# Optimization experiments

Hardware: AMD Instinct MI355X
Metric: run time of the kernel (lower is better)

## Reference

```python
import jax, jax.numpy as jnp
import numpy as np

B, I, A_IN = 32, 32, 16     # batch, input capsules, input atoms
OD, OA = 10, 16             # output_dim (classes), output_atoms
H, W = 12, 12               # spatial grid
NUM_ROUTING = 3


def _squash(t):
    # squash over atom dim (axis=2): x/|x| * |x|^2/(1+|x|^2) = x*|x|/(1+|x|^2)
    norm = jnp.linalg.norm(t, axis=2, keepdims=True)
    return t * norm / (1.0 + norm * norm)


def setup_inputs() -> dict:
    key = jax.random.key(0)
    k1, k2 = jax.random.split(key)
    x = jax.random.normal(k1, (B, I, A_IN, H, W), dtype=jnp.float32)
    # torch weight: (I, A_IN, OD*OA, 1, 1), init N(0, 0.1)
    weight = 0.1 * jax.random.normal(k2, (I, A_IN, OD * OA), dtype=jnp.float32)
    # torch bias: (OD, OA, 1, 1), init const 0.1
    bias = jnp.full((OD, OA, 1, 1), 0.1, dtype=jnp.float32)
    return {"x": x, "weight": weight, "bias": bias}


def reference(x, weight, bias):
    # votes: sum over input atoms -> [B, I, OD*OA, H, W] -> [B, I, OD, OA, H, W]
    votes = jnp.einsum("biahw,iak->bikhw", x, weight)
    votes = votes.reshape(B, I, OD, OA, H, W)
    biases = jnp.broadcast_to(bias, (OD, OA, H, W))

    # Dynamic routing. In the original, logits carry no gradient (built from
    # .data), so intermediate iterations are fully stop-gradient.
    votes_sg = jax.lax.stop_gradient(votes)
    logits = jnp.zeros((B, I, OD, H, W), dtype=votes.dtype)
    activation = None
    for i in range(NUM_ROUTING):
        route = jax.nn.softmax(logits, axis=2)  # softmax over output_dim
        v = votes if i == NUM_ROUTING - 1 else votes_sg
        preact = jnp.einsum("bidhw,bidahw->bdahw", route, v) + biases
        activation = _squash(preact)  # [B, OD, OA, H, W]
        if i < NUM_ROUTING - 1:
            # agreement (dot over atoms) updates logits
            logits = logits + jnp.einsum(
                "bidahw,bdahw->bidhw", votes_sg, jax.lax.stop_gradient(activation)
            )
    return activation
```

## Files before the change

### kernel.cpp

```cpp
#include <hip/hip_runtime.h>
#include <math.h>

#define NB 32
#define NI 32
#define NA 16
#define NOD 10
#define NOA 16
#define NK 160
#define NHW 144
#define NROUT 3
#define P 2
#define NTHREADS 512
#define SVLD 168

__device__ __forceinline__ unsigned short f2bf(float f) {
    unsigned b = __builtin_bit_cast(unsigned, f);
    b += 0x7fffu + ((b >> 16) & 1u);
    return (unsigned short)(b >> 16);
}
__device__ __forceinline__ float bf2f(unsigned short u) {
    return __builtin_bit_cast(float, (unsigned)u << 16);
}
__device__ __forceinline__ float bf_lo(unsigned d) {
    return __builtin_bit_cast(float, d << 16);
}
__device__ __forceinline__ float bf_hi(unsigned d) {
    return __builtin_bit_cast(float, d & 0xffff0000u);
}

__global__ __launch_bounds__(NTHREADS)
void capsule_routing_kernel(const float* __restrict__ x,
                            const float* __restrict__ weight,
                            const float* __restrict__ bias,
                            float* __restrict__ out)
{
    __shared__ float sx[NI][NA][P];
    __shared__ unsigned short sv[P * NI * SVLD];
    __shared__ float slog[P][NI][NOD];
    __shared__ float srt[P][NI][NOD];
    __shared__ float sact[P][NOD][NOA];

    const int bk  = blockIdx.x;
    const int b   = bk / (NHW / P);
    const int hw0 = (bk % (NHW / P)) * P;
    const int tid = threadIdx.x;

#define SVIDX(p, i, k) (((p) * NI + (i)) * SVLD + (k))

    if (tid < NI * NA) {
        const int i = tid >> 4;
        const int a = tid & (NA - 1);
        const float2 v = *reinterpret_cast<const float2*>(
            x + (size_t)((b * NI + i) * NA + a) * NHW + hw0);
        sx[i][a][0] = v.x;
        sx[i][a][1] = v.y;
    }
    {
        float* lf = &slog[0][0][0];
        for (int j = tid; j < P * NI * NOD; j += NTHREADS) lf[j] = 0.0f;
    }
    __syncthreads();

    for (int j = tid; j < NI * (NK / 4); j += NTHREADS) {
        const int i  = j / (NK / 4);
        const int k0 = (j - i * (NK / 4)) * 4;
        const float4* wp = reinterpret_cast<const float4*>(
            weight + (size_t)i * NA * NK + k0);
        float4 a0 = make_float4(0.f, 0.f, 0.f, 0.f);
        float4 a1 = make_float4(0.f, 0.f, 0.f, 0.f);
#pragma unroll
        for (int a = 0; a < NA; ++a) {
            const float4 w4 = wp[a * (NK / 4)];
            const float2 xa = *reinterpret_cast<const float2*>(&sx[i][a][0]);
            a0.x = fmaf(xa.x, w4.x, a0.x); a0.y = fmaf(xa.x, w4.y, a0.y);
            a0.z = fmaf(xa.x, w4.z, a0.z); a0.w = fmaf(xa.x, w4.w, a0.w);
            a1.x = fmaf(xa.y, w4.x, a1.x); a1.y = fmaf(xa.y, w4.y, a1.y);
            a1.z = fmaf(xa.y, w4.z, a1.z); a1.w = fmaf(xa.y, w4.w, a1.w);
        }
        ushort4 s0 = make_ushort4(f2bf(a0.x), f2bf(a0.y), f2bf(a0.z), f2bf(a0.w));
        ushort4 s1 = make_ushort4(f2bf(a1.x), f2bf(a1.y), f2bf(a1.z), f2bf(a1.w));
        *reinterpret_cast<ushort4*>(&sv[SVIDX(0, i, k0)]) = s0;
        *reinterpret_cast<ushort4*>(&sv[SVIDX(1, i, k0)]) = s1;
    }
    __syncthreads();

    for (int it = 0; it < NROUT; ++it) {
        if (tid < P * NI) {
            const int p = tid >> 5;
            const int i = tid & 31;
            float m = slog[p][i][0];
#pragma unroll
            for (int od = 1; od < NOD; ++od) m = fmaxf(m, slog[p][i][od]);
            float e[NOD];
            float s = 0.0f;
#pragma unroll
            for (int od = 0; od < NOD; ++od) {
                e[od] = __expf(slog[p][i][od] - m);
                s += e[od];
            }
            const float inv = 1.0f / s;
#pragma unroll
            for (int od = 0; od < NOD; ++od) srt[p][i][od] = e[od] * inv;
        }
        __syncthreads();

        if (tid < P * NK) {
            const int p  = tid / NK;
            const int k  = tid - p * NK;
            const int od = k >> 4;
            const int oa = k & (NOA - 1);
            float acc = bias[k];
            const unsigned short* svp = &sv[SVIDX(p, 0, k)];
#pragma unroll
            for (int i = 0; i < NI; ++i)
                acc = fmaf(srt[p][i][od], bf2f(svp[i * SVLD]), acc);
            float ss = acc * acc;
#pragma unroll
            for (int m = 1; m < NOA; m <<= 1)
                ss += __shfl_xor(ss, m, NOA);
            const float scale = sqrtf(ss) / (1.0f + ss);
            sact[p][od][oa] = acc * scale;
        }
        __syncthreads();

        if (it < NROUT - 1) {
            for (int j = tid; j < P * NI * NOD; j += NTHREADS) {
                const int p  = j / (NI * NOD);
                const int r  = j - p * (NI * NOD);
                const int od = r >> 5;
                const int i  = r & 31;
                const uint4 d0 = *reinterpret_cast<const uint4*>(
                    &sv[SVIDX(p, i, od * NOA)]);
                const uint4 d1 = *reinterpret_cast<const uint4*>(
                    &sv[SVIDX(p, i, od * NOA + 8)]);
                const float* ap = &sact[p][od][0];
                float acc;
                acc  = bf_lo(d0.x) * ap[0];
                acc = fmaf(bf_hi(d0.x), ap[1], acc);
                acc = fmaf(bf_lo(d0.y), ap[2], acc);
                acc = fmaf(bf_hi(d0.y), ap[3], acc);
                acc = fmaf(bf_lo(d0.z), ap[4], acc);
                acc = fmaf(bf_hi(d0.z), ap[5], acc);
                acc = fmaf(bf_lo(d0.w), ap[6], acc);
                acc = fmaf(bf_hi(d0.w), ap[7], acc);
                acc = fmaf(bf_lo(d1.x), ap[8], acc);
                acc = fmaf(bf_hi(d1.x), ap[9], acc);
                acc = fmaf(bf_lo(d1.y), ap[10], acc);
                acc = fmaf(bf_hi(d1.y), ap[11], acc);
                acc = fmaf(bf_lo(d1.z), ap[12], acc);
                acc = fmaf(bf_hi(d1.z), ap[13], acc);
                acc = fmaf(bf_lo(d1.w), ap[14], acc);
                acc = fmaf(bf_hi(d1.w), ap[15], acc);
                slog[p][i][od] += acc;
            }
            __syncthreads();
        }
    }

    __syncthreads();
    if (tid < NK) {
        const int od = tid >> 4;
        const int oa = tid & (NOA - 1);
        const float2 v = make_float2(sact[0][od][oa], sact[1][od][oa]);
        *reinterpret_cast<float2*>(out + (size_t)(b * NK + tid) * NHW + hw0) = v;
    }
}

extern "C" void kernel_launch(void* const* d_in, const int* in_sizes, int n_in,
                              void* d_out, int out_size, void* d_ws, size_t ws_size,
                              hipStream_t stream) {
    const float* x      = (const float*)d_in[0];
    const float* weight = (const float*)d_in[1];
    const float* bias   = (const float*)d_in[2];
    float* out          = (float*)d_out;

    const int nblocks = NB * (NHW / P);
    capsule_routing_kernel<<<nblocks, NTHREADS, 0, stream>>>(x, weight, bias, out);
}
```

Before: 47.92 us.

## Split vote computation into separate kernel writing bf16 votes to workspace

Splits the fused kernel in two. A votes kernel computes all votes once per (capsule, batch, half-grid), loading each weight slice into shared memory and writing bf16 votes to the workspace. A routing kernel then reads four spatial positions per block and keeps the routing logits in registers. This removes the redundant per-block weight reads of the fused version, but adds a global round trip of about 47 MB of bf16 votes and a second launch. A fallback to the original fused kernel is kept for when the workspace is too small.

```diff
diff --git a/kernel.cpp b/kernel.cpp
--- a/kernel.cpp
+++ b/kernel.cpp
@@ -9,9 +9,8 @@
 #define NK 160
 #define NHW 144
 #define NROUT 3
-#define P 2
-#define NTHREADS 512
-#define SVLD 168
+#define NROWS (NB*NHW)
+#define VOTES_BYTES ((size_t)NI * NROWS * NK * 2)
 
 __device__ __forceinline__ unsigned short f2bf(float f) {
     unsigned b = __builtin_bit_cast(unsigned, f);
@@ -28,24 +27,194 @@
     return __builtin_bit_cast(float, d & 0xffff0000u);
 }
 
-__global__ __launch_bounds__(NTHREADS)
-void capsule_routing_kernel(const float* __restrict__ x,
-                            const float* __restrict__ weight,
-                            const float* __restrict__ bias,
-                            float* __restrict__ out)
+__global__ __launch_bounds__(256)
+void votes_kernel(const float* __restrict__ x,
+                  const float* __restrict__ weight,
+                  unsigned short* __restrict__ votes)
 {
-    __shared__ float sx[NI][NA][P];
+    __shared__ float sw[NA * NK];
+    __shared__ float sxv[NA * 72];
+
+    const int i   = blockIdx.x >> 6;
+    const int b   = (blockIdx.x >> 1) & 31;
+    const int hw0 = (blockIdx.x & 1) * 72;
+    const int tid = threadIdx.x;
+
+    {
+        const float4* src = reinterpret_cast<const float4*>(weight + (size_t)i * NA * NK);
+        float4* dst = reinterpret_cast<float4*>(sw);
+        for (int j = tid; j < NA * NK / 4; j += 256) dst[j] = src[j];
+    }
+    {
+        const float* xb = x + ((size_t)(b * NI + i) * NA) * NHW + hw0;
+        for (int j = tid; j < NA * 18; j += 256) {
+            const int a = j / 18, c = j % 18;
+            *reinterpret_cast<float4*>(&sxv[a * 72 + c * 4]) =
+                *reinterpret_cast<const float4*>(xb + a * NHW + c * 4);
+        }
+    }
+    __syncthreads();
+
+    unsigned short* vbase = votes + ((size_t)i * NROWS + b * NHW + hw0) * NK;
+    for (int t = tid; t < 72 * 40; t += 256) {
+        const int kq  = (t >> 2) % 40;
+        const int hwl = (t & 3) + ((t / 160) << 2);
+        const int k0  = kq * 4;
+        float4 acc = make_float4(0.f, 0.f, 0.f, 0.f);
+#pragma unroll
+        for (int a = 0; a < NA; ++a) {
+            const float  xv = sxv[a * 72 + hwl];
+            const float4 w4 = *reinterpret_cast<const float4*>(&sw[a * NK + k0]);
+            acc.x = fmaf(xv, w4.x, acc.x);
+            acc.y = fmaf(xv, w4.y, acc.y);
+            acc.z = fmaf(xv, w4.z, acc.z);
+            acc.w = fmaf(xv, w4.w, acc.w);
+        }
+        const ushort4 s = make_ushort4(f2bf(acc.x), f2bf(acc.y), f2bf(acc.z), f2bf(acc.w));
+        *reinterpret_cast<ushort4*>(vbase + (size_t)hwl * NK + k0) = s;
+    }
+}
+
+#define P 4
+#define SVLD 168
+
+__global__ __launch_bounds__(512)
+void routing_kernel(const unsigned short* __restrict__ votes,
+                    const float* __restrict__ bias,
+                    float* __restrict__ out)
+{
     __shared__ unsigned short sv[P * NI * SVLD];
-    __shared__ float slog[P][NI][NOD];
     __shared__ float srt[P][NI][NOD];
     __shared__ float sact[P][NOD][NOA];
 
+    const int row0 = blockIdx.x * P;
+    const int tid  = threadIdx.x;
+
+    {
+        const uint4* src = reinterpret_cast<const uint4*>(votes);
+        for (int u = tid; u < NI * P * 20; u += 512) {
+            const int i = u / (P * 20);
+            const int r = u % (P * 20);
+            const int p = r / 20;
+            const int c = r % 20;
+            *reinterpret_cast<uint4*>(&sv[(p * NI + i) * SVLD + c * 8]) =
+                src[(size_t)(i * NROWS + row0 + p) * 20 + c];
+        }
+    }
+
+    float lg[NOD];
+#pragma unroll
+    for (int od = 0; od < NOD; ++od) lg[od] = 0.f;
+    const int pown = tid >> 5;
+    const int iown = tid & 31;
+    __syncthreads();
+
+    for (int it = 0; it < NROUT; ++it) {
+        if (tid < P * NI) {
+            float m = lg[0];
+#pragma unroll
+            for (int od = 1; od < NOD; ++od) m = fmaxf(m, lg[od]);
+            float e[NOD];
+            float s = 0.f;
+#pragma unroll
+            for (int od = 0; od < NOD; ++od) {
+                e[od] = __expf(lg[od] - m);
+                s += e[od];
+            }
+            const float inv = 1.f / s;
+#pragma unroll
+            for (int od = 0; od < NOD; ++od) srt[pown][iown][od] = e[od] * inv;
+        }
+        __syncthreads();
+
+        for (int j = tid; j < P * NK; j += 512) {
+            const int p  = j / NK;
+            const int k  = j - p * NK;
+            const int od = k >> 4;
+            const int oa = k & 15;
+            float acc = bias[k];
+            const unsigned short* svp = &sv[p * NI * SVLD + k];
+#pragma unroll
+            for (int i = 0; i < NI; ++i)
+                acc = fmaf(srt[p][i][od], bf2f(svp[i * SVLD]), acc);
+            float ss = acc * acc;
+#pragma unroll
+            for (int m = 1; m < NOA; m <<= 1)
+                ss += __shfl_xor(ss, m, NOA);
+            const float scale = sqrtf(ss) / (1.f + ss);
+            sact[p][od][oa] = acc * scale;
+        }
+        __syncthreads();
+
+        if (it < NROUT - 1) {
+            for (int j = tid; j < P * NI * NOD; j += 512) {
+                const int p  = j / (NI * NOD);
+                const int r  = j - p * (NI * NOD);
+                const int od = r >> 5;
+                const int i  = r & 31;
+                const uint4 d0 = *reinterpret_cast<const uint4*>(
+                    &sv[(p * NI + i) * SVLD + od * NOA]);
+                const uint4 d1 = *reinterpret_cast<const uint4*>(
+                    &sv[(p * NI + i) * SVLD + od * NOA + 8]);
+                const float* ap = &sact[p][od][0];
+                float acc;
+                acc  = bf_lo(d0.x) * ap[0];
+                acc = fmaf(bf_hi(d0.x), ap[1], acc);
+                acc = fmaf(bf_lo(d0.y), ap[2], acc);
+                acc = fmaf(bf_hi(d0.y), ap[3], acc);
+                acc = fmaf(bf_lo(d0.z), ap[4], acc);
+                acc = fmaf(bf_hi(d0.z), ap[5], acc);
+                acc = fmaf(bf_lo(d0.w), ap[6], acc);
+                acc = fmaf(bf_hi(d0.w), ap[7], acc);
+                acc = fmaf(bf_lo(d1.x), ap[8], acc);
+                acc = fmaf(bf_hi(d1.x), ap[9], acc);
+                acc = fmaf(bf_lo(d1.y), ap[10], acc);
+                acc = fmaf(bf_hi(d1.y), ap[11], acc);
+                acc = fmaf(bf_lo(d1.z), ap[12], acc);
+                acc = fmaf(bf_hi(d1.z), ap[13], acc);
+                acc = fmaf(bf_lo(d1.w), ap[14], acc);
+                acc = fmaf(bf_hi(d1.w), ap[15], acc);
+                srt[p][i][od] = acc;
+            }
+            __syncthreads();
+            if (tid < P * NI) {
+#pragma unroll
+                for (int od = 0; od < NOD; ++od) lg[od] += srt[pown][iown][od];
+            }
+        }
+    }
+
+    if (tid < NK) {
+        const int b  = row0 / NHW;
+        const int hw = row0 % NHW;
+        const int od = tid >> 4;
+        const int oa = tid & 15;
+        const float4 v = make_float4(sact[0][od][oa], sact[1][od][oa],
+                                     sact[2][od][oa], sact[3][od][oa]);
+        *reinterpret_cast<float4*>(out + ((size_t)b * NK + tid) * NHW + hw) = v;
+    }
+}
+
+#define FP 2
+#define FSVLD 168
+
+__global__ __launch_bounds__(512)
+void capsule_fallback_kernel(const float* __restrict__ x,
+                             const float* __restrict__ weight,
+                             const float* __restrict__ bias,
+                             float* __restrict__ out)
+{
+    __shared__ float sx[NI][NA][FP];
+    __shared__ unsigned short sv[FP * NI * FSVLD];
+    __shared__ float slog[FP][NI][NOD];
+    __shared__ float srt[FP][NI][NOD];
+    __shared__ float sact[FP][NOD][NOA];
+
     const int bk  = blockIdx.x;
-    const int b   = bk / (NHW / P);
-    const int hw0 = (bk % (NHW / P)) * P;
+    const int b   = bk / (NHW / FP);
+    const int hw0 = (bk % (NHW / FP)) * FP;
     const int tid = threadIdx.x;
-
-#define SVIDX(p, i, k) (((p) * NI + (i)) * SVLD + (k))
+#define FSVIDX(p, i, k) (((p) * NI + (i)) * FSVLD + (k))
 
     if (tid < NI * NA) {
         const int i = tid >> 4;
@@ -57,15 +226,14 @@
     }
     {
         float* lf = &slog[0][0][0];
-        for (int j = tid; j < P * NI * NOD; j += NTHREADS) lf[j] = 0.0f;
-    }
-    __syncthreads();
-
-    for (int j = tid; j < NI * (NK / 4); j += NTHREADS) {
+        for (int j = tid; j < FP * NI * NOD; j += 512) lf[j] = 0.0f;
+    }
+    __syncthreads();
+
+    for (int j = tid; j < NI * (NK / 4); j += 512) {
         const int i  = j / (NK / 4);
         const int k0 = (j - i * (NK / 4)) * 4;
-        const float4* wp = reinterpret_cast<const float4*>(
-            weight + (size_t)i * NA * NK + k0);
+        const float4* wp = reinterpret_cast<const float4*>(weight + (size_t)i * NA * NK + k0);
         float4 a0 = make_float4(0.f, 0.f, 0.f, 0.f);
         float4 a1 = make_float4(0.f, 0.f, 0.f, 0.f);
 #pragma unroll
@@ -79,13 +247,13 @@
         }
         ushort4 s0 = make_ushort4(f2bf(a0.x), f2bf(a0.y), f2bf(a0.z), f2bf(a0.w));
         ushort4 s1 = make_ushort4(f2bf(a1.x), f2bf(a1.y), f2bf(a1.z), f2bf(a1.w));
-        *reinterpret_cast<ushort4*>(&sv[SVIDX(0, i, k0)]) = s0;
-        *reinterpret_cast<ushort4*>(&sv[SVIDX(1, i, k0)]) = s1;
+        *reinterpret_cast<ushort4*>(&sv[FSVIDX(0, i, k0)]) = s0;
+        *reinterpret_cast<ushort4*>(&sv[FSVIDX(1, i, k0)]) = s1;
     }
     __syncthreads();
 
     for (int it = 0; it < NROUT; ++it) {
-        if (tid < P * NI) {
+        if (tid < FP * NI) {
             const int p = tid >> 5;
             const int i = tid & 31;
             float m = slog[p][i][0];
@@ -104,16 +272,16 @@
         }
         __syncthreads();
 
-        if (tid < P * NK) {
+        if (tid < FP * NK) {
             const int p  = tid / NK;
             const int k  = tid - p * NK;
             const int od = k >> 4;
             const int oa = k & (NOA - 1);
             float acc = bias[k];
-            const unsigned short* svp = &sv[SVIDX(p, 0, k)];
+            const unsigned short* svp = &sv[FSVIDX(p, 0, k)];
 #pragma unroll
             for (int i = 0; i < NI; ++i)
-                acc = fmaf(srt[p][i][od], bf2f(svp[i * SVLD]), acc);
+                acc = fmaf(srt[p][i][od], bf2f(svp[i * FSVLD]), acc);
             float ss = acc * acc;
 #pragma unroll
             for (int m = 1; m < NOA; m <<= 1)
@@ -124,15 +292,13 @@
         __syncthreads();
 
         if (it < NROUT - 1) {
-            for (int j = tid; j < P * NI * NOD; j += NTHREADS) {
+            for (int j = tid; j < FP * NI * NOD; j += 512) {
                 const int p  = j / (NI * NOD);
                 const int r  = j - p * (NI * NOD);
                 const int od = r >> 5;
                 const int i  = r & 31;
-                const uint4 d0 = *reinterpret_cast<const uint4*>(
-                    &sv[SVIDX(p, i, od * NOA)]);
-                const uint4 d1 = *reinterpret_cast<const uint4*>(
-                    &sv[SVIDX(p, i, od * NOA + 8)]);
+                const uint4 d0 = *reinterpret_cast<const uint4*>(&sv[FSVIDX(p, i, od * NOA)]);
+                const uint4 d1 = *reinterpret_cast<const uint4*>(&sv[FSVIDX(p, i, od * NOA + 8)]);
                 const float* ap = &sact[p][od][0];
                 float acc;
                 acc  = bf_lo(d0.x) * ap[0];
@@ -174,6 +340,11 @@
     const float* bias   = (const float*)d_in[2];
     float* out          = (float*)d_out;
 
-    const int nblocks = NB * (NHW / P);
-    capsule_routing_kernel<<<nblocks, NTHREADS, 0, stream>>>(x, weight, bias, out);
-}
+    if (ws_size >= VOTES_BYTES) {
+        unsigned short* votes = (unsigned short*)d_ws;
+        votes_kernel<<<NI * NB * 2, 256, 0, stream>>>(x, weight, votes);
+        routing_kernel<<<NROWS / P, 512, 0, stream>>>(votes, bias, out);
+    } else {
+        capsule_fallback_kernel<<<NB * (NHW / FP), 512, 0, stream>>>(x, weight, bias, out);
+    }
+}
```

New measurement: 62.60 us. +30.6%, slower.

## Assign one wavefront per spatial position and route with wave-level sync

Applied to the files above, without the earlier changes.

Each block now handles 4 spatial positions with 256 threads, one 64-lane wave per position. Routing logits live in registers and every routing step syncs with wave barriers instead of block-wide __syncthreads. The vote computation reuses each weight load across 4 positions instead of 2, which halves weight traffic per output. The risk is fewer blocks, and wave-barrier correctness relies on each wave touching only its own shared-memory slices.

```diff
diff --git a/kernel.cpp b/kernel.cpp
--- a/kernel.cpp
+++ b/kernel.cpp
@@ -9,8 +9,7 @@
 #define NK 160
 #define NHW 144
 #define NROUT 3
-#define P 2
-#define NTHREADS 512
+#define NROWS (NB*NHW)
 #define SVLD 168
 
 __device__ __forceinline__ unsigned short f2bf(float f) {
@@ -18,9 +17,6 @@
     b += 0x7fffu + ((b >> 16) & 1u);
     return (unsigned short)(b >> 16);
 }
-__device__ __forceinline__ float bf2f(unsigned short u) {
-    return __builtin_bit_cast(float, (unsigned)u << 16);
-}
 __device__ __forceinline__ float bf_lo(unsigned d) {
     return __builtin_bit_cast(float, d << 16);
 }
@@ -28,141 +24,181 @@
     return __builtin_bit_cast(float, d & 0xffff0000u);
 }
 
-__global__ __launch_bounds__(NTHREADS)
-void capsule_routing_kernel(const float* __restrict__ x,
-                            const float* __restrict__ weight,
-                            const float* __restrict__ bias,
-                            float* __restrict__ out)
+__global__ __launch_bounds__(256)
+void capsule_fused_kernel(const float* __restrict__ x,
+                          const float* __restrict__ weight,
+                          const float* __restrict__ bias,
+                          float* __restrict__ out)
 {
-    __shared__ float sx[NI][NA][P];
-    __shared__ unsigned short sv[P * NI * SVLD];
-    __shared__ float slog[P][NI][NOD];
-    __shared__ float srt[P][NI][NOD];
-    __shared__ float sact[P][NOD][NOA];
-
-    const int bk  = blockIdx.x;
-    const int b   = bk / (NHW / P);
-    const int hw0 = (bk % (NHW / P)) * P;
-    const int tid = threadIdx.x;
-
-#define SVIDX(p, i, k) (((p) * NI + (i)) * SVLD + (k))
-
-    if (tid < NI * NA) {
-        const int i = tid >> 4;
-        const int a = tid & (NA - 1);
-        const float2 v = *reinterpret_cast<const float2*>(
-            x + (size_t)((b * NI + i) * NA + a) * NHW + hw0);
-        sx[i][a][0] = v.x;
-        sx[i][a][1] = v.y;
-    }
+    __shared__ unsigned short sv[4][NI][SVLD];
+    __shared__ __align__(16) float pool[2048];
+    float* const srt_f  = pool;
+    float* const sact_f = pool + 4 * NOD * 33;
+
+    const int tid  = threadIdx.x;
+    const int w    = tid >> 6;
+    const int l    = tid & 63;
+    const int b    = blockIdx.x / (NHW / 4);
+    const int hw0  = (blockIdx.x % (NHW / 4)) * 4;
+
     {
-        float* lf = &slog[0][0][0];
-        for (int j = tid; j < P * NI * NOD; j += NTHREADS) lf[j] = 0.0f;
+        const float* xb = x + ((size_t)b * NI * NA) * NHW + hw0;
+        for (int j = tid; j < NI * NA; j += 256) {
+            const float4 v = *reinterpret_cast<const float4*>(xb + (size_t)j * NHW);
+            *reinterpret_cast<float4*>(&pool[j * 4]) = v;
+        }
     }
     __syncthreads();
 
-    for (int j = tid; j < NI * (NK / 4); j += NTHREADS) {
-        const int i  = j / (NK / 4);
-        const int k0 = (j - i * (NK / 4)) * 4;
+    for (int j = tid; j < NI * 40; j += 256) {
+        const int i  = j / 40;
+        const int kq = j - i * 40;
+        const int k0 = kq * 4;
         const float4* wp = reinterpret_cast<const float4*>(
             weight + (size_t)i * NA * NK + k0);
         float4 a0 = make_float4(0.f, 0.f, 0.f, 0.f);
         float4 a1 = make_float4(0.f, 0.f, 0.f, 0.f);
+        float4 a2 = make_float4(0.f, 0.f, 0.f, 0.f);
+        float4 a3 = make_float4(0.f, 0.f, 0.f, 0.f);
 #pragma unroll
         for (int a = 0; a < NA; ++a) {
-            const float4 w4 = wp[a * (NK / 4)];
-            const float2 xa = *reinterpret_cast<const float2*>(&sx[i][a][0]);
+            const float4 w4 = wp[(size_t)a * 40];
+            const float4 xa = *reinterpret_cast<const float4*>(&pool[(i * NA + a) * 4]);
             a0.x = fmaf(xa.x, w4.x, a0.x); a0.y = fmaf(xa.x, w4.y, a0.y);
             a0.z = fmaf(xa.x, w4.z, a0.z); a0.w = fmaf(xa.x, w4.w, a0.w);
             a1.x = fmaf(xa.y, w4.x, a1.x); a1.y = fmaf(xa.y, w4.y, a1.y);
             a1.z = fmaf(xa.y, w4.z, a1.z); a1.w = fmaf(xa.y, w4.w, a1.w);
-        }
-        ushort4 s0 = make_ushort4(f2bf(a0.x), f2bf(a0.y), f2bf(a0.z), f2bf(a0.w));
-        ushort4 s1 = make_ushort4(f2bf(a1.x), f2bf(a1.y), f2bf(a1.z), f2bf(a1.w));
-        *reinterpret_cast<ushort4*>(&sv[SVIDX(0, i, k0)]) = s0;
-        *reinterpret_cast<ushort4*>(&sv[SVIDX(1, i, k0)]) = s1;
-    }
+            a2.x = fmaf(xa.z, w4.x, a2.x); a2.y = fmaf(xa.z, w4.y, a2.y);
+            a2.z = fmaf(xa.z, w4.z, a2.z); a2.w = fmaf(xa.z, w4.w, a2.w);
+            a3.x = fmaf(xa.w, w4.x, a3.x); a3.y = fmaf(xa.w, w4.y, a3.y);
+            a3.z = fmaf(xa.w, w4.z, a3.z); a3.w = fmaf(xa.w, w4.w, a3.w);
+        }
+        *reinterpret_cast<ushort4*>(&sv[0][i][k0]) =
+            make_ushort4(f2bf(a0.x), f2bf(a0.y), f2bf(a0.z), f2bf(a0.w));
+        *reinterpret_cast<ushort4*>(&sv[1][i][k0]) =
+            make_ushort4(f2bf(a1.x), f2bf(a1.y), f2bf(a1.z), f2bf(a1.w));
+        *reinterpret_cast<ushort4*>(&sv[2][i][k0]) =
+            make_ushort4(f2bf(a2.x), f2bf(a2.y), f2bf(a2.z), f2bf(a2.w));
+        *reinterpret_cast<ushort4*>(&sv[3][i][k0]) =
+            make_ushort4(f2bf(a3.x), f2bf(a3.y), f2bf(a3.z), f2bf(a3.w));
+    }
+
+    const float2 b0 = *reinterpret_cast<const float2*>(bias + 2 * l);
+    float2 b1 = make_float2(0.f, 0.f);
+    if (l < 16) b1 = *reinterpret_cast<const float2*>(bias + 128 + 2 * l);
+
+    float lg[NOD];
+#pragma unroll
+    for (int od = 0; od < NOD; ++od) lg[od] = 0.f;
+    const int iown = l & 31;
+
     __syncthreads();
 
     for (int it = 0; it < NROUT; ++it) {
-        if (tid < P * NI) {
-            const int p = tid >> 5;
-            const int i = tid & 31;
-            float m = slog[p][i][0];
-#pragma unroll
-            for (int od = 1; od < NOD; ++od) m = fmaxf(m, slog[p][i][od]);
+        {
+            float m = lg[0];
+#pragma unroll
+            for (int od = 1; od < NOD; ++od) m = fmaxf(m, lg[od]);
             float e[NOD];
-            float s = 0.0f;
+            float s = 0.f;
 #pragma unroll
             for (int od = 0; od < NOD; ++od) {
-                e[od] = __expf(slog[p][i][od] - m);
+                e[od] = __expf(lg[od] - m);
                 s += e[od];
             }
-            const float inv = 1.0f / s;
-#pragma unroll
-            for (int od = 0; od < NOD; ++od) srt[p][i][od] = e[od] * inv;
-        }
-        __syncthreads();
-
-        if (tid < P * NK) {
-            const int p  = tid / NK;
-            const int k  = tid - p * NK;
-            const int od = k >> 4;
-            const int oa = k & (NOA - 1);
-            float acc = bias[k];
-            const unsigned short* svp = &sv[SVIDX(p, 0, k)];
-#pragma unroll
-            for (int i = 0; i < NI; ++i)
-                acc = fmaf(srt[p][i][od], bf2f(svp[i * SVLD]), acc);
-            float ss = acc * acc;
-#pragma unroll
-            for (int m = 1; m < NOA; m <<= 1)
-                ss += __shfl_xor(ss, m, NOA);
-            const float scale = sqrtf(ss) / (1.0f + ss);
-            sact[p][od][oa] = acc * scale;
-        }
-        __syncthreads();
+            const float inv = 1.f / s;
+            if (l < 32) {
+#pragma unroll
+                for (int od = 0; od < NOD; ++od)
+                    srt_f[(w * NOD + od) * 33 + iown] = e[od] * inv;
+            }
+        }
+        __builtin_amdgcn_wave_barrier();
+
+        {
+            const int od0 = l >> 3;
+            float a0 = b0.x, a1 = b0.y;
+#pragma unroll
+            for (int i = 0; i < NI; ++i) {
+                const unsigned d = *reinterpret_cast<const unsigned*>(&sv[w][i][2 * l]);
+                const float r = srt_f[(w * NOD + od0) * 33 + i];
+                a0 = fmaf(r, bf_lo(d), a0);
+                a1 = fmaf(r, bf_hi(d), a1);
+            }
+            float ss = a0 * a0 + a1 * a1;
+            ss += __shfl_xor(ss, 1, 8);
+            ss += __shfl_xor(ss, 2, 8);
+            ss += __shfl_xor(ss, 4, 8);
+            const float sc = sqrtf(ss) / (1.f + ss);
+            *reinterpret_cast<float2*>(&sact_f[w * 164 + 2 * l]) =
+                make_float2(a0 * sc, a1 * sc);
+
+            if (l < 16) {
+                const int od1 = 8 + (l >> 3);
+                float c0 = b1.x, c1 = b1.y;
+#pragma unroll
+                for (int i = 0; i < NI; ++i) {
+                    const unsigned d = *reinterpret_cast<const unsigned*>(&sv[w][i][128 + 2 * l]);
+                    const float r = srt_f[(w * NOD + od1) * 33 + i];
+                    c0 = fmaf(r, bf_lo(d), c0);
+                    c1 = fmaf(r, bf_hi(d), c1);
+                }
+                float s2 = c0 * c0 + c1 * c1;
+                s2 += __shfl_xor(s2, 1, 8);
+                s2 += __shfl_xor(s2, 2, 8);
+                s2 += __shfl_xor(s2, 4, 8);
+                const float sc2 = sqrtf(s2) / (1.f + s2);
+                *reinterpret_cast<float2*>(&sact_f[w * 164 + 128 + 2 * l]) =
+                    make_float2(c0 * sc2, c1 * sc2);
+            }
+        }
+        __builtin_amdgcn_wave_barrier();
 
         if (it < NROUT - 1) {
-            for (int j = tid; j < P * NI * NOD; j += NTHREADS) {
-                const int p  = j / (NI * NOD);
-                const int r  = j - p * (NI * NOD);
-                const int od = r >> 5;
-                const int i  = r & 31;
-                const uint4 d0 = *reinterpret_cast<const uint4*>(
-                    &sv[SVIDX(p, i, od * NOA)]);
-                const uint4 d1 = *reinterpret_cast<const uint4*>(
-                    &sv[SVIDX(p, i, od * NOA + 8)]);
-                const float* ap = &sact[p][od][0];
+#pragma unroll
+            for (int r = 0; r < 5; ++r) {
+                const int t  = l + 64 * r;
+                const int i  = t & 31;
+                const int od = t >> 5;
+                const uint4 d0 = *reinterpret_cast<const uint4*>(&sv[w][i][od * NOA]);
+                const uint4 d1 = *reinterpret_cast<const uint4*>(&sv[w][i][od * NOA + 8]);
+                const float* ap = &sact_f[w * 164 + od * NOA];
+                const float4 c0 = *reinterpret_cast<const float4*>(ap + 0);
+                const float4 c1 = *reinterpret_cast<const float4*>(ap + 4);
+                const float4 c2 = *reinterpret_cast<const float4*>(ap + 8);
+                const float4 c3 = *reinterpret_cast<const float4*>(ap + 12);
                 float acc;
-                acc  = bf_lo(d0.x) * ap[0];
-                acc = fmaf(bf_hi(d0.x), ap[1], acc);
-                acc = fmaf(bf_lo(d0.y), ap[2], acc);
-                acc = fmaf(bf_hi(d0.y), ap[3], acc);
-                acc = fmaf(bf_lo(d0.z), ap[4], acc);
-                acc = fmaf(bf_hi(d0.z), ap[5], acc);
-                acc = fmaf(bf_lo(d0.w), ap[6], acc);
-                acc = fmaf(bf_hi(d0.w), ap[7], acc);
-                acc = fmaf(bf_lo(d1.x), ap[8], acc);
-                acc = fmaf(bf_hi(d1.x), ap[9], acc);
-                acc = fmaf(bf_lo(d1.y), ap[10], acc);
-                acc = fmaf(bf_hi(d1.y), ap[11], acc);
-                acc = fmaf(bf_lo(d1.z), ap[12], acc);
-                acc = fmaf(bf_hi(d1.z), ap[13], acc);
-                acc = fmaf(bf_lo(d1.w), ap[14], acc);
-                acc = fmaf(bf_hi(d1.w), ap[15], acc);
-                slog[p][i][od] += acc;
-            }
-            __syncthreads();
+                acc  = bf_lo(d0.x) * c0.x;
+                acc = fmaf(bf_hi(d0.x), c0.y, acc);
+                acc = fmaf(bf_lo(d0.y), c0.z, acc);
+                acc = fmaf(bf_hi(d0.y), c0.w, acc);
+                acc = fmaf(bf_lo(d0.z), c1.x, acc);
+                acc = fmaf(bf_hi(d0.z), c1.y, acc);
+                acc = fmaf(bf_lo(d0.w), c1.z, acc);
+                acc = fmaf(bf_hi(d0.w), c1.w, acc);
+                acc = fmaf(bf_lo(d1.x), c2.x, acc);
+                acc = fmaf(bf_hi(d1.x), c2.y, acc);
+                acc = fmaf(bf_lo(d1.y), c2.z, acc);
+                acc = fmaf(bf_hi(d1.y), c2.w, acc);
+                acc = fmaf(bf_lo(d1.z), c3.x, acc);
+                acc = fmaf(bf_hi(d1.z), c3.y, acc);
+                acc = fmaf(bf_lo(d1.w), c3.z, acc);
+                acc = fmaf(bf_hi(d1.w), c3.w, acc);
+                srt_f[(w * NOD + od) * 33 + i] = acc;
+            }
+            __builtin_amdgcn_wave_barrier();
+#pragma unroll
+            for (int od = 0; od < NOD; ++od)
+                lg[od] += srt_f[(w * NOD + od) * 33 + iown];
+            __builtin_amdgcn_wave_barrier();
         }
     }
 
     __syncthreads();
     if (tid < NK) {
-        const int od = tid >> 4;
-        const int oa = tid & (NOA - 1);
-        const float2 v = make_float2(sact[0][od][oa], sact[1][od][oa]);
-        *reinterpret_cast<float2*>(out + (size_t)(b * NK + tid) * NHW + hw0) = v;
+        const float4 v = make_float4(sact_f[0 * 164 + tid], sact_f[1 * 164 + tid],
+                                     sact_f[2 * 164 + tid], sact_f[3 * 164 + tid]);
+        *reinterpret_cast<float4*>(out + ((size_t)b * NK + tid) * NHW + hw0) = v;
     }
 }
 
@@ -174,6 +210,5 @@
     const float* bias   = (const float*)d_in[2];
     float* out          = (float*)d_out;
 
-    const int nblocks = NB * (NHW / P);
-    capsule_routing_kernel<<<nblocks, NTHREADS, 0, stream>>>(x, weight, bias, out);
-}
+    capsule_fused_kernel<<<NROWS / 4, 256, 0, stream>>>(x, weight, bias, out);
+}
```

Measured after the change: 43.54 us. 1.1x faster.
